# Performance work log

Hardware: AMD Instinct MI355X
Metric: run time of the kernel (lower is better)

The kernel has to match this reference:

```python
import jax, jax.numpy as jnp
import numpy as np
from jax import lax

LAGS = np.array([1, 2, 3, 4, 5, 6, 7, 14, 21, 28])
MAX_LAG = int(LAGS.max())
N_LAGS = len(LAGS)
HID = 512
EMB_ROWS, EMB_DIM = 12, 5
BATCH, CTX, HOR = 128, 720, 168
T0 = CTX + HOR + MAX_LAG  # 916
IN_DIM = 1 + N_LAGS + 1 + EMB_DIM  # target + lags + log-scale + seq-cat embedding = 17


def _lstm_cell(x, h, c, Wih, Whh, bih, bhh):
    g = x @ Wih.T + h @ Whh.T + bih + bhh
    i, f, gg, o = jnp.split(g, 4, axis=-1)  # torch gate order i,f,g,o
    c = jax.nn.sigmoid(f) * c + jax.nn.sigmoid(i) * jnp.tanh(gg)
    h = jax.nn.sigmoid(o) * jnp.tanh(c)
    return h, c


def _run_layer(xs, params):
    Bn = xs.shape[0]
    z = jnp.zeros((Bn, HID), xs.dtype)
    def step(hc, x):
        h, c = _lstm_cell(x, hc[0], hc[1], *params)
        return (h, c), h
    hc, ys = lax.scan(step, (z, z), jnp.swapaxes(xs, 0, 1))
    return jnp.swapaxes(ys, 0, 1), hc


def _forward(X, pad_mask, emb, W_ih0, W_hh0, b_ih0, b_hh0,
             W_ih1, W_hh1, b_ih1, b_hh1, W_head, b_head, H, C):
    Bn = X.shape[0]
    p0 = (W_ih0, W_hh0, b_ih0, b_hh0)
    p1 = (W_ih1, W_hh1, b_ih1, b_hh1)
    X = X.at[:, -H:, 0].set(0.0)
    past = X[:, :X.shape[1] - H, 0][:, ::-1]  # [B, C+MAX_LAG], newest first
    Xt = X[:, MAX_LAG:]                       # [B, T, 2], T = C + H
    mask = pad_mask[:, MAX_LAG:][:, :C].astype(X.dtype)
    scale = (jnp.abs(Xt[:, :C, 0]) * mask).sum(1) / jnp.clip(mask.sum(1), 1.0)
    scale = jnp.maximum(scale, 1e-10)         # [B]
    tgt = Xt[:, :, 0] / scale[:, None]        # scaled target
    past = past / scale[:, None]
    # context lag features: value at context step t is past[C-1-t]; lag l -> past[C-1-t+l]
    idx = (C - 1 - np.arange(C))[:, None] + LAGS[None, :]  # [C, N_LAGS], static
    lags_ctx = past[:, idx]                                # [B, C, N_LAGS]
    logscale = jnp.log(scale)[:, None]                     # [B, 1]
    seq_emb = emb[Xt[:, :, 1].astype(jnp.int32)]           # [B, T, EMB_DIM]
    x_ctx = jnp.concatenate([
        tgt[:, :C, None], lags_ctx,
        jnp.broadcast_to(logscale[:, None, :], (Bn, C, 1)),
        seq_emb[:, :C]], 2)                                # [B, C, IN_DIM]
    o1, hc1 = _run_layer(x_ctx, p0)
    o2, hc2 = _run_layer(o1, p1)
    y_ctx = o2 @ W_head.T + b_head                         # [B, C, 1]
    # per-step static decode features (log-scale + seq-cat embedding)
    feat_dec = jnp.concatenate([
        jnp.broadcast_to(logscale[:, None, :], (Bn, H - 1, 1)),
        seq_emb[:, C:C + H - 1]], 2)                       # [B, H-1, 1+EMB_DIM]
    lag_idx = LAGS - 1
    def dec_step(carry, feat):
        h1, c1, h2, c2, buf, prev = carry
        lag_t = buf[:, lag_idx]                            # [B, N_LAGS]
        # step input is clone().detach()'d in the original -> stop_gradient
        x_t = lax.stop_gradient(jnp.concatenate([prev[:, None], lag_t, feat], 1))
        h1, c1 = _lstm_cell(x_t, h1, c1, *p0)
        h2, c2 = _lstm_cell(h1, h2, c2, *p1)
        o = h2 @ W_head.T + b_head                         # [B, 1]
        buf = jnp.concatenate([prev[:, None], buf[:, :-1]], 1)
        return (h1, c1, h2, c2, buf, o[:, 0]), o
    carry0 = (hc1[0], hc1[1], hc2[0], hc2[1], past[:, :MAX_LAG], y_ctx[:, -1, 0])
    _, y_dec = lax.scan(dec_step, carry0, jnp.swapaxes(feat_dec, 0, 1))
    y_hat = jnp.concatenate([y_ctx, jnp.swapaxes(y_dec, 0, 1)], 1)  # [B, C+H-1, 1]
    return y_hat * scale[:, None, None]


def setup_inputs():
    key = jax.random.key(0)
    ks = jax.random.split(key, 10)
    s = 0.05
    tgt = jax.random.normal(ks[0], (BATCH, T0, 1), jnp.float32)
    cat = jax.random.randint(ks[1], (BATCH, T0, 1), 0, EMB_ROWS).astype(jnp.float32)
    return {
        "X": jnp.concatenate([tgt, cat], 2),
        "pad_mask": jnp.ones((BATCH, T0), dtype=bool),
        "emb": jax.random.normal(ks[2], (EMB_ROWS, EMB_DIM), jnp.float32) * s,
        "W_ih0": jax.random.normal(ks[3], (4 * HID, IN_DIM), jnp.float32) * s,
        "W_hh0": jax.random.normal(ks[4], (4 * HID, HID), jnp.float32) * s,
        "b_ih0": jnp.zeros((4 * HID,), jnp.float32),
        "b_hh0": jnp.zeros((4 * HID,), jnp.float32),
        "W_ih1": jax.random.normal(ks[5], (4 * HID, HID), jnp.float32) * s,
        "W_hh1": jax.random.normal(ks[6], (4 * HID, HID), jnp.float32) * s,
        "b_ih1": jnp.zeros((4 * HID,), jnp.float32),
        "b_hh1": jnp.zeros((4 * HID,), jnp.float32),
        "W_head": jax.random.normal(ks[7], (1, HID), jnp.float32) * s,
        "b_head": jnp.zeros((1,), jnp.float32),
        "H": HOR,
        "context_length": CTX,
    }


def reference(X, pad_mask, emb, W_ih0, W_hh0, b_ih0, b_hh0,
              W_ih1, W_hh1, b_ih1, b_hh1, W_head, b_head, H, context_length):
    return _forward(X, pad_mask, emb, W_ih0, W_hh0, b_ih0, b_hh0,
                    W_ih1, W_hh1, b_ih1, b_hh1, W_head, b_head, H, context_length)
```

## Files before the change

### kernel.cpp

```cpp
#include <hip/hip_runtime.h>
#include <math.h>


#define CTXL   720
#define MAXLAG 28
#define TT0    916
#define NSTEP  887
#define OUTW   887
#define HS2    (128 * 256)

typedef _Float16 h2v   __attribute__((ext_vector_type(2)));
typedef _Float16 half8 __attribute__((ext_vector_type(8)));
typedef float    f32x4 __attribute__((ext_vector_type(4)));

struct Prm {
  const float* __restrict__ Wih0; const float* __restrict__ Whh0;
  const float* __restrict__ bih0; const float* __restrict__ bhh0;
  const float* __restrict__ Wih1; const float* __restrict__ Whh1;
  const float* __restrict__ bih1; const float* __restrict__ bhh1;
  const float* __restrict__ Whead; const float* __restrict__ bhead;
  const float* __restrict__ scale; const float* __restrict__ ls;
  const float* __restrict__ V; const float* __restrict__ embf;
  unsigned* __restrict__ H0; unsigned* __restrict__ H1;
  float* __restrict__ Ypart;
  float* __restrict__ out;
  int* __restrict__ bar;
};

__device__ __forceinline__ void stb(float* p, float v) {
  __hip_atomic_store(p, v, __ATOMIC_RELAXED, __HIP_MEMORY_SCOPE_AGENT);
}
__device__ __forceinline__ void stbu(unsigned* p, unsigned v) {
  __hip_atomic_store(p, v, __ATOMIC_RELAXED, __HIP_MEMORY_SCOPE_AGENT);
}
__device__ __forceinline__ float ldb(const float* p) {
  return __hip_atomic_load(p, __ATOMIC_RELAXED, __HIP_MEMORY_SCOPE_AGENT);
}
__device__ __forceinline__ int ldbi(const int* p) {
  return __hip_atomic_load(p, __ATOMIC_RELAXED, __HIP_MEMORY_SCOPE_AGENT);
}
__device__ __forceinline__ uint2 ldbu2(const unsigned* p) {
  union { unsigned long long u; uint2 v; } cv;
  cv.u = __hip_atomic_load((const unsigned long long*)p, __ATOMIC_RELAXED,
                           __HIP_MEMORY_SCOPE_AGENT);
  return cv.v;
}
__device__ __forceinline__ float sigm(float x) {
  return __builtin_amdgcn_rcpf(1.f + __expf(-x));
}
__device__ __forceinline__ float tanh_f(float x) {
  return fmaf(2.f, __builtin_amdgcn_rcpf(1.f + __expf(-2.f * x)), -1.f);
}
__device__ __forceinline__ unsigned packh2(float a, float b) {
  union { h2v h; unsigned u; } cv;
  cv.h = h2v{(_Float16)a, (_Float16)b};
  return cv.u;
}

__global__ void prep_kernel(const float* __restrict__ X, const float* __restrict__ emb,
                            float* __restrict__ scale, float* __restrict__ ls,
                            float* __restrict__ V, float* __restrict__ embf,
                            unsigned* __restrict__ zb , int* __restrict__ bar)
{
    const int bid = blockIdx.x, tid = threadIdx.x;
    if (bid < 128) {
        const int b = bid;
        __shared__ float sred[256];
        __shared__ float s_scale;
        float p = 0.f;
        for (int t = tid; t < CTXL; t += 256)
            p += fabsf(X[(size_t)(b * TT0 + MAXLAG + t) * 2]);
        sred[tid] = p; __syncthreads();
        for (int s = 128; s > 0; s >>= 1) {
            if (tid < s) sred[tid] += sred[tid + s];
            __syncthreads();
        }
        if (tid == 0) {
            float sc = fmaxf(sred[0] / (float)CTXL, 1e-10f);
            s_scale = sc; scale[b] = sc; ls[b] = logf(sc);
        }
        __syncthreads();
        const float sc = s_scale;
        for (int j = tid; j < TT0 - 168; j += 256)
            V[(size_t)j * 128 + b] = X[(size_t)(b * TT0 + j) * 2] / sc;
        for (int t = tid; t < NSTEP; t += 256) {
            int cc = (int)X[(size_t)(b * TT0 + MAXLAG + t) * 2 + 1];
            #pragma unroll
            for (int d = 0; d < 5; ++d)
                embf[((size_t)t * 5 + d) * 128 + b] = emb[cc * 5 + d];
        }
    } else {
        const int ZT = 4 * HS2;
        for (int idx = (bid - 128) * 256 + tid; idx < ZT; idx += 128 * 256)
            zb[idx] = 0u;
        if (bid == 128) { bar[tid] = 0; bar[256 + tid] = 0; }
    }
}

#define STAGE(LDSBUF, GSRC) { _Pragma("unroll")                               \
    for (int r_ = 0; r_ < 2; ++r_) {                                          \
      const int ch_ = tid + r_ * 512;                                         \
      const int sl_ = ch_ >> 6, c_ = ch_ & 63;                                \
      const unsigned* gp_ = (GSRC) + (size_t)(S0 + sl_) * 256 + c_ * 4;       \
      const uint2 a_ = ldbu2(gp_), b_ = ldbu2(gp_ + 2);                       \
      *(uint4*)&(LDSBUF)[sl_ * 256 + ((c_ * 4) ^ ((sl_ & 7) << 2))] =         \
          make_uint4(a_.x, a_.y, b_.x, b_.y); } }

#define MMPASS(D) { _Pragma("unroll")                                         \
    for (int t_ = 0; t_ < 16; ++t_) {                                         \
      union { uint4 u; half8 h; } b0_, b1_;                                   \
      b0_.u = *(const uint4*)&h0lds[ar * 256 + ((t_ * 16 + akg * 4) ^ xsw)];  \
      b1_.u = *(const uint4*)&h1lds[ar * 256 + ((t_ * 16 + akg * 4) ^ xsw)];  \
      D = __builtin_amdgcn_mfma_f32_16x16x32_f16(awA[t_], b0_.h, D, 0, 0, 0); \
      D = __builtin_amdgcn_mfma_f32_16x16x32_f16(awB[t_], b1_.h, D, 0, 0, 0); } }

#define XDOT(G, XF) { const int ub_ = (T * 4 + akg) * 68;                     \
    _Pragma("unroll")                                                         \
    for (int q_ = 0; q_ < 4; ++q_) { float xd_ = b4[q_];                      \
      _Pragma("unroll")                                                       \
      for (int j_ = 0; j_ < 17; ++j_)                                         \
          xd_ = fmaf(sX0[ub_ + q_ * 17 + j_], (XF)[j_], xd_);                 \
      (G)[q_] += xd_; } }

#define OUTWRITE(PAR, STEP) {                                                 \
    float v_ = ldb(&p.Ypart[(size_t)(PAR) * 4096 + (S0 + (tid >> 5)) * 32 + (tid & 31)]); \
    v_ += __shfl_xor(v_, 1, 64); v_ += __shfl_xor(v_, 2, 64);                 \
    v_ += __shfl_xor(v_, 4, 64); v_ += __shfl_xor(v_, 8, 64);                 \
    v_ += __shfl_xor(v_, 16, 64);                                             \
    if ((l & 31) == 0)                                                        \
        stb(&p.out[(size_t)(S0 + (tid >> 5)) * OUTW + (STEP)],                \
            (v_ + bh_all) * sc_my); }

__global__ __launch_bounds__(512, 2) void deepar_persist(Prm p)
{
    const int tid = threadIdx.x, blk = blockIdx.x;
    const int ublk = blk >> 3, grp = blk & 7;
    const int U0 = ublk * 16, S0 = grp * 16;
    const int l = tid & 63, wv = tid >> 6;
    const int ar = l & 15, akg = l >> 4;
    const bool isL0 = (wv < 4);
    const int T = isL0 ? wv : (wv - 4);
    const int u = U0 + T * 4 + akg;
    const int sg = S0 + ar;
    const int xsw = (ar & 7) << 2;

    __shared__ unsigned h0lds[16 * 256];
    __shared__ unsigned h1lds[16 * 256];
    __shared__ float sX0[16 * 68];
    __shared__ float sYring[168 * 16];
    __shared__ float sYp[4][16];

    half8 awA[16], awB[16];
    {
        const int grow = ((ar & 3) << 9) + U0 + T * 4 + (ar >> 2);
        const float* srcA = isL0 ? p.Whh0 : p.Wih1;
        #pragma unroll
        for (int t = 0; t < 16; ++t) {
            #pragma unroll
            for (int j = 0; j < 8; ++j) {
                const int k = t * 32 + akg * 8 + j;
                awA[t][j] = (_Float16)srcA[(size_t)grow * 512 + k];
                awB[t][j] = isL0 ? (_Float16)0.f
                                 : (_Float16)p.Whh1[(size_t)grow * 512 + k];
            }
        }
    }
    for (int idx = tid; idx < 1088; idx += 512) {
        const int ul = idx / 68, r = idx % 68;
        const int q = r / 17, j = r % 17;
        sX0[idx] = p.Wih0[((q << 9) + U0 + ul) * 17 + j];
    }

    float cc = 0.f;
    float b4[4];
    float lsv = 0.f, whm = 0.f;
    if (isL0) {
        #pragma unroll
        for (int q = 0; q < 4; ++q)
            b4[q] = p.bih0[(q << 9) + u] + p.bhh0[(q << 9) + u];
        lsv = p.ls[sg];
    } else {
        #pragma unroll
        for (int q = 0; q < 4; ++q)
            b4[q] = p.bih1[(q << 9) + u] + p.bhh1[(q << 9) + u];
        whm = p.Whead[u];
    }
    const float bh_all = p.bhead[0];
    const float sc_my = p.scale[S0 + (tid >> 5)];
    __syncthreads();

    f32x4 g0c = {0.f, 0.f, 0.f, 0.f};
    int ph = 0;
    const int LG[10] = {1, 2, 3, 4, 5, 6, 7, 14, 21, 28};
    int* gctr = p.bar + grp * 64;

    auto gbar = [&]() {
        asm volatile("s_waitcnt vmcnt(0)" ::: "memory");
        __syncthreads();
        ++ph;
        if (wv == 7) {
            if (l == 0)
                __hip_atomic_fetch_add(&gctr[(ublk & 3) * 16], 1,
                                       __ATOMIC_RELAXED, __HIP_MEMORY_SCOPE_AGENT);
            const int target = 32 * ph;
            for (;;) {
                int v = (l < 4) ? ldbi(&gctr[l * 16]) : 0;
                v += __shfl_xor(v, 1, 64); v += __shfl_xor(v, 2, 64);
                if (__shfl(v, 0, 64) >= target) break;
                __builtin_amdgcn_s_sleep(1);
            }
        }
        __syncthreads();
    };

    for (int P = 0; P <= CTXL; ++P) {
        if (P >= 2 && ublk == (P & 31)) OUTWRITE(P & 1, P - 2);

        STAGE(h0lds, p.H0 + (size_t)((P - 1) & 1) * HS2);
        STAGE(h1lds, p.H1 + (size_t)(P & 1) * HS2);
        __syncthreads();

        f32x4 d = {0.f, 0.f, 0.f, 0.f};
        MMPASS(d);

        if (isL0) {
            if (P < CTXL) {
                float xf[17];
                xf[0] = p.V[(size_t)(MAXLAG + P) * 128 + sg];
                #pragma unroll
                for (int j = 0; j < 10; ++j)
                    xf[1 + j] = p.V[(size_t)(MAXLAG + P - LG[j]) * 128 + sg];
                xf[11] = lsv;
                #pragma unroll
                for (int dd = 0; dd < 5; ++dd)
                    xf[12 + dd] = p.embf[((size_t)P * 5 + dd) * 128 + sg];
                float g[4] = { d[0], d[1], d[2], d[3] };
                XDOT(g, xf);
                const float ig = sigm(g[0]), fg = sigm(g[1]);
                const float gt = tanh_f(g[2]), og = sigm(g[3]);
                cc = fg * cc + ig * gt;
                const float h = og * tanh_f(cc);
                const float other = __shfl_xor(h, 16, 64);
                if (!(akg & 1))
                    stbu(&p.H0[(size_t)(P & 1) * HS2 + (size_t)sg * 256
                               + ublk * 8 + T * 2 + (akg >> 1)],
                         packh2(h, other));
            } else {
                g0c = d;
            }
        } else if (P >= 1) {
            float g[4] = { d[0] + b4[0], d[1] + b4[1], d[2] + b4[2], d[3] + b4[3] };
            const float ig = sigm(g[0]), fg = sigm(g[1]);
            const float gt = tanh_f(g[2]), og = sigm(g[3]);
            cc = fg * cc + ig * gt;
            const float h = og * tanh_f(cc);
            const float other = __shfl_xor(h, 16, 64);
            if (!(akg & 1))
                stbu(&p.H1[(size_t)((P - 1) & 1) * HS2 + (size_t)sg * 256
                           + ublk * 8 + T * 2 + (akg >> 1)],
                     packh2(h, other));
            float yp = whm * h;
            yp += __shfl_xor(yp, 16, 64);
            yp += __shfl_xor(yp, 32, 64);
            if (akg == 0) sYp[T][ar] = yp;
        }
        __syncthreads();
        if (P >= 1 && tid < 16) {
            const float ys = (sYp[0][tid] + sYp[1][tid]) + (sYp[2][tid] + sYp[3][tid]);
            stb(&p.Ypart[(size_t)((P - 1) & 1) * 4096 + (S0 + tid) * 32 + ublk], ys);
        }
        gbar();
    }

    for (int t = CTXL; t < NSTEP; ++t) {
        {
            STAGE(h1lds, p.H1 + (size_t)((t - 1) & 1) * HS2);

            const int par = (t - 1) & 1;
            float v = ldb(&p.Ypart[(size_t)par * 4096 + (S0 + (tid >> 5)) * 32 + (tid & 31)]);
            v += __shfl_xor(v, 1, 64); v += __shfl_xor(v, 2, 64);
            v += __shfl_xor(v, 4, 64); v += __shfl_xor(v, 8, 64);
            v += __shfl_xor(v, 16, 64);
            if ((l & 31) == 0) {
                const float yv = v + bh_all;
                sYring[(t - CTXL) * 16 + (tid >> 5)] = yv;
                if (ublk == (t & 31))
                    stb(&p.out[(size_t)(S0 + (tid >> 5)) * OUTW + (t - 1)], yv * sc_my);
            }
            __syncthreads();

            if (isL0) {
                const float yprev = sYring[(t - CTXL) * 16 + ar];
                float xf[17];
                xf[0] = yprev;
                #pragma unroll
                for (int j = 0; j < 10; ++j) {
                    const int uu = t - LG[j];
                    const int ri = (uu - CTXL) < 0 ? 0 : (uu - CTXL);
                    xf[1 + j] = (uu < CTXL) ? p.V[(size_t)(MAXLAG + uu) * 128 + sg]
                                            : sYring[ri * 16 + ar];
                }
                xf[11] = lsv;
                #pragma unroll
                for (int dd = 0; dd < 5; ++dd)
                    xf[12 + dd] = p.embf[((size_t)t * 5 + dd) * 128 + sg];
                float g[4] = { g0c[0], g0c[1], g0c[2], g0c[3] };
                XDOT(g, xf);
                const float ig = sigm(g[0]), fg = sigm(g[1]);
                const float gt = tanh_f(g[2]), og = sigm(g[3]);
                cc = fg * cc + ig * gt;
                const float h = og * tanh_f(cc);
                const float other = __shfl_xor(h, 16, 64);
                if (!(akg & 1))
                    stbu(&p.H0[(size_t)(t & 1) * HS2 + (size_t)sg * 256
                               + ublk * 8 + T * 2 + (akg >> 1)],
                         packh2(h, other));
            }
            gbar();
        }
        {
            STAGE(h0lds, p.H0 + (size_t)(t & 1) * HS2);
            __syncthreads();

            f32x4 d = {0.f, 0.f, 0.f, 0.f};
            MMPASS(d);

            if (isL0) {
                g0c = d;
            } else {
                float g[4] = { d[0] + b4[0], d[1] + b4[1], d[2] + b4[2], d[3] + b4[3] };
                const float ig = sigm(g[0]), fg = sigm(g[1]);
                const float gt = tanh_f(g[2]), og = sigm(g[3]);
                cc = fg * cc + ig * gt;
                const float h = og * tanh_f(cc);
                const float other = __shfl_xor(h, 16, 64);
                if (!(akg & 1))
                    stbu(&p.H1[(size_t)(t & 1) * HS2 + (size_t)sg * 256
                               + ublk * 8 + T * 2 + (akg >> 1)],
                         packh2(h, other));
                float yp = whm * h;
                yp += __shfl_xor(yp, 16, 64);
                yp += __shfl_xor(yp, 32, 64);
                if (akg == 0) sYp[T][ar] = yp;
            }
            __syncthreads();
            if (tid < 16) {
                const float ys = (sYp[0][tid] + sYp[1][tid]) + (sYp[2][tid] + sYp[3][tid]);
                stb(&p.Ypart[(size_t)(t & 1) * 4096 + (S0 + tid) * 32 + ublk], ys);
            }
            gbar();
        }
    }

    if (ublk == ((NSTEP - 1) & 31)) OUTWRITE(0, NSTEP - 1);
}

extern "C" void kernel_launch(void* const* d_in, const int* in_sizes, int n_in,
                              void* d_out, int out_size, void* d_ws, size_t ws_size,
                              hipStream_t stream)
{
    (void)in_sizes; (void)n_in; (void)out_size; (void)ws_size;
    const float* X   = (const float*)d_in[0];
    const float* emb = (const float*)d_in[2];
    Prm prm;
    prm.Wih0 = (const float*)d_in[3];
    prm.Whh0 = (const float*)d_in[4];
    prm.bih0 = (const float*)d_in[5];
    prm.bhh0 = (const float*)d_in[6];
    prm.Wih1 = (const float*)d_in[7];
    prm.Whh1 = (const float*)d_in[8];
    prm.bih1 = (const float*)d_in[9];
    prm.bhh1 = (const float*)d_in[10];
    prm.Whead = (const float*)d_in[11];
    prm.bhead = (const float*)d_in[12];
    float* out = (float*)d_out;

    float* ws    = (float*)d_ws;
    float* scale = ws;
    float* ls    = scale + 128;
    float* V     = ls + 128;
    float* embf  = V + 748 * 128;
    unsigned* H0 = (unsigned*)(embf + (size_t)888 * 5 * 128);
    unsigned* H1 = H0 + 2 * HS2;
    float* Ypart = (float*)(H1 + 2 * HS2);
    int*   bar   = (int*)(Ypart + 2 * 128 * 32);

    hipLaunchKernelGGL(prep_kernel, dim3(256), dim3(256), 0, stream,
                       X, emb, scale, ls, V, embf, H0, bar);

    prm.scale = scale; prm.ls = ls; prm.V = V; prm.embf = embf;
    prm.H0 = H0; prm.H1 = H1; prm.Ypart = Ypart; prm.out = out;
    prm.bar = bar;

    void* args[] = { &prm };
    hipLaunchCooperativeKernel((void*)deepar_persist, dim3(256), dim3(512),
                               args, 0, stream);
}
```

Before: 6.737 ms.

## Skip zero-weight MFMAs for layer0 waves and split grid barrier arrive/wait

```diff
diff --git a/kernel.cpp b/kernel.cpp
--- a/kernel.cpp
+++ b/kernel.cpp
@@ -106,13 +106,19 @@
       *(uint4*)&(LDSBUF)[sl_ * 256 + ((c_ * 4) ^ ((sl_ & 7) << 2))] =         \
           make_uint4(a_.x, a_.y, b_.x, b_.y); } }
 
-#define MMPASS(D) { _Pragma("unroll")                                         \
+#define MMPASS_L1(D) { _Pragma("unroll")                                      \
     for (int t_ = 0; t_ < 16; ++t_) {                                         \
       union { uint4 u; half8 h; } b0_, b1_;                                   \
       b0_.u = *(const uint4*)&h0lds[ar * 256 + ((t_ * 16 + akg * 4) ^ xsw)];  \
       b1_.u = *(const uint4*)&h1lds[ar * 256 + ((t_ * 16 + akg * 4) ^ xsw)];  \
       D = __builtin_amdgcn_mfma_f32_16x16x32_f16(awA[t_], b0_.h, D, 0, 0, 0); \
       D = __builtin_amdgcn_mfma_f32_16x16x32_f16(awB[t_], b1_.h, D, 0, 0, 0); } }
+
+#define MMPASS_L0(D) { _Pragma("unroll")                                      \
+    for (int t_ = 0; t_ < 16; ++t_) {                                         \
+      union { uint4 u; half8 h; } b0_;                                        \
+      b0_.u = *(const uint4*)&h0lds[ar * 256 + ((t_ * 16 + akg * 4) ^ xsw)];  \
+      D = __builtin_amdgcn_mfma_f32_16x16x32_f16(awA[t_], b0_.h, D, 0, 0, 0); } }
 
 #define XDOT(G, XF) { const int ub_ = (T * 4 + akg) * 68;                     \
     _Pragma("unroll")                                                         \
@@ -131,7 +137,7 @@
         stb(&p.out[(size_t)(S0 + (tid >> 5)) * OUTW + (STEP)],                \
             (v_ + bh_all) * sc_my); }
 
-__global__ __launch_bounds__(512, 2) void deepar_persist(Prm p)
+__global__ __launch_bounds__(512, 1) void deepar_persist(Prm p)
 {
     const int tid = threadIdx.x, blk = blockIdx.x;
     const int ublk = blk >> 3, grp = blk & 7;
@@ -160,8 +166,16 @@
             for (int j = 0; j < 8; ++j) {
                 const int k = t * 32 + akg * 8 + j;
                 awA[t][j] = (_Float16)srcA[(size_t)grow * 512 + k];
-                awB[t][j] = isL0 ? (_Float16)0.f
-                                 : (_Float16)p.Whh1[(size_t)grow * 512 + k];
+            }
+        }
+        if (!isL0) {
+            #pragma unroll
+            for (int t = 0; t < 16; ++t) {
+                #pragma unroll
+                for (int j = 0; j < 8; ++j) {
+                    const int k = t * 32 + akg * 8 + j;
+                    awB[t][j] = (_Float16)p.Whh1[(size_t)grow * 512 + k];
+                }
             }
         }
     }
@@ -194,14 +208,16 @@
     const int LG[10] = {1, 2, 3, 4, 5, 6, 7, 14, 21, 28};
     int* gctr = p.bar + grp * 64;
 
-    auto gbar = [&]() {
+    auto gbar_arrive = [&]() {
         asm volatile("s_waitcnt vmcnt(0)" ::: "memory");
         __syncthreads();
         ++ph;
+        if (wv == 7 && l == 0)
+            __hip_atomic_fetch_add(&gctr[(ublk & 3) * 16], 1,
+                                   __ATOMIC_RELAXED, __HIP_MEMORY_SCOPE_AGENT);
+    };
+    auto gbar_wait = [&]() {
         if (wv == 7) {
-            if (l == 0)
-                __hip_atomic_fetch_add(&gctr[(ublk & 3) * 16], 1,
-                                       __ATOMIC_RELAXED, __HIP_MEMORY_SCOPE_AGENT);
             const int target = 32 * ph;
             for (;;) {
                 int v = (l < 4) ? ldbi(&gctr[l * 16]) : 0;
@@ -214,26 +230,27 @@
     };
 
     for (int P = 0; P <= CTXL; ++P) {
-        if (P >= 2 && ublk == (P & 31)) OUTWRITE(P & 1, P - 2);
-
         STAGE(h0lds, p.H0 + (size_t)((P - 1) & 1) * HS2);
         STAGE(h1lds, p.H1 + (size_t)(P & 1) * HS2);
+
+        float xf[17];
+        if (isL0 && P < CTXL) {
+            xf[0] = p.V[(size_t)(MAXLAG + P) * 128 + sg];
+            #pragma unroll
+            for (int j = 0; j < 10; ++j)
+                xf[1 + j] = p.V[(size_t)(MAXLAG + P - LG[j]) * 128 + sg];
+            xf[11] = lsv;
+            #pragma unroll
+            for (int dd = 0; dd < 5; ++dd)
+                xf[12 + dd] = p.embf[((size_t)P * 5 + dd) * 128 + sg];
+        }
         __syncthreads();
 
         f32x4 d = {0.f, 0.f, 0.f, 0.f};
-        MMPASS(d);
+        if (isL0) { MMPASS_L0(d); } else { MMPASS_L1(d); }
 
         if (isL0) {
             if (P < CTXL) {
-                float xf[17];
-                xf[0] = p.V[(size_t)(MAXLAG + P) * 128 + sg];
-                #pragma unroll
-                for (int j = 0; j < 10; ++j)
-                    xf[1 + j] = p.V[(size_t)(MAXLAG + P - LG[j]) * 128 + sg];
-                xf[11] = lsv;
-                #pragma unroll
-                for (int dd = 0; dd < 5; ++dd)
-                    xf[12 + dd] = p.embf[((size_t)P * 5 + dd) * 128 + sg];
                 float g[4] = { d[0], d[1], d[2], d[3] };
                 XDOT(g, xf);
                 const float ig = sigm(g[0]), fg = sigm(g[1]);
@@ -269,7 +286,9 @@
             const float ys = (sYp[0][tid] + sYp[1][tid]) + (sYp[2][tid] + sYp[3][tid]);
             stb(&p.Ypart[(size_t)((P - 1) & 1) * 4096 + (S0 + tid) * 32 + ublk], ys);
         }
-        gbar();
+        gbar_arrive();
+        if (P >= 2 && ublk == (P & 31)) OUTWRITE(P & 1, P - 2);
+        gbar_wait();
     }
 
     for (int t = CTXL; t < NSTEP; ++t) {
@@ -316,14 +335,15 @@
                                + ublk * 8 + T * 2 + (akg >> 1)],
                          packh2(h, other));
             }
-            gbar();
+            gbar_arrive();
+            gbar_wait();
         }
         {
             STAGE(h0lds, p.H0 + (size_t)(t & 1) * HS2);
             __syncthreads();
 
             f32x4 d = {0.f, 0.f, 0.f, 0.f};
-            MMPASS(d);
+            if (isL0) { MMPASS_L0(d); } else { MMPASS_L1(d); }
 
             if (isL0) {
                 g0c = d;
@@ -348,7 +368,8 @@
                 const float ys = (sYp[0][tid] + sYp[1][tid]) + (sYp[2][tid] + sYp[3][tid]);
                 stb(&p.Ypart[(size_t)(t & 1) * 4096 + (S0 + tid) * 32 + ublk], ys);
             }
-            gbar();
+            gbar_arrive();
+            gbar_wait();
         }
     }
 
```

Result: faster. 6.152 ms (-8.7%).
